# Kernel optimization log

Measured on AMD Instinct MI355X. Metric: run time of the kernel, lower is better.

Reference implementation:

```python
import jax, jax.numpy as jnp
import numpy as np

B, N, DIN, D, L, H = 8, 1024, 768, 384, 6, 12
HD = D // H
STD = 0.02
EPS = 1e-5


def setup_inputs() -> dict:
    key = jax.random.key(0)
    ks = jax.random.split(key, 24)
    inp = {}
    inp["x"] = jax.random.normal(ks[0], (B, N, DIN), jnp.float32)
    inp["height_ids"] = jax.random.randint(ks[1], (B, N), 0, 48)
    inp["width_ids"] = jax.random.randint(ks[2], (B, N), 0, 48)
    inp["target_mask"] = jax.random.randint(ks[3], (B, N), 0, 2).astype(bool)
    inp["sequence_ids"] = jnp.sort(jax.random.randint(ks[4], (B, N), 0, 8), axis=-1)
    inp["sequence_mask"] = (jax.random.randint(ks[5], (B, N), 0, 10) > 8)
    inp["r"] = 0
    # parameters (weights stored [in, out]; y = x @ W + b)
    inp["embed_w"] = jax.random.normal(ks[6], (DIN, D), jnp.float32) * STD
    inp["embed_b"] = jnp.zeros((D,), jnp.float32)
    inp["h_embed"] = jax.random.normal(ks[7], (48, D), jnp.float32) * STD
    inp["w_embed"] = jax.random.normal(ks[8], (48, D), jnp.float32) * STD
    inp["mask_token"] = jax.random.normal(ks[9], (D,), jnp.float32) * STD
    rescale = (1.0 / jnp.sqrt(2.0 * (jnp.arange(L) + 1.0))).astype(jnp.float32)
    inp["norm1_w"] = jnp.ones((L, D), jnp.float32)
    inp["norm1_b"] = jnp.zeros((L, D), jnp.float32)
    inp["ls1"] = 1e-5 * jnp.ones((L, D), jnp.float32)
    inp["qkv_w"] = jax.random.normal(ks[10], (L, D, 3 * D), jnp.float32) * STD
    inp["qkv_b"] = jnp.zeros((L, 3 * D), jnp.float32)
    inp["proj_w"] = jax.random.normal(ks[11], (L, D, D), jnp.float32) * STD * rescale[:, None, None]
    inp["proj_b"] = jnp.zeros((L, D), jnp.float32)
    inp["norm2_w"] = jnp.ones((L, D), jnp.float32)
    inp["norm2_b"] = jnp.zeros((L, D), jnp.float32)
    inp["fc1_w"] = jax.random.normal(ks[12], (L, D, 4 * D), jnp.float32) * STD
    inp["fc1_b"] = jnp.zeros((L, 4 * D), jnp.float32)
    inp["fc2_w"] = jax.random.normal(ks[13], (L, 4 * D, D), jnp.float32) * STD * rescale[:, None, None]
    inp["fc2_b"] = jnp.zeros((L, D), jnp.float32)
    inp["ls2"] = 1e-5 * jnp.ones((L, D), jnp.float32)
    inp["pnorm_w"] = jnp.ones((D,), jnp.float32)
    inp["pnorm_b"] = jnp.zeros((D,), jnp.float32)
    inp["pproj_w"] = jax.random.normal(ks[14], (D, DIN), jnp.float32) * STD
    inp["pproj_b"] = jnp.zeros((DIN,), jnp.float32)
    return inp


def _layernorm(x, w, b):
    mu = jnp.mean(x, axis=-1, keepdims=True)
    var = jnp.mean(jnp.square(x - mu), axis=-1, keepdims=True)
    return (x - mu) * jax.lax.rsqrt(var + EPS) * w + b


def _attention(x, attn_mask, qkv_w, qkv_b, proj_w, proj_b):
    # x: [B,N,D]; attn_mask: [B,1,N,N] True where attention is disallowed
    qkv = (x @ qkv_w + qkv_b).reshape(B, N, 3, H, HD).transpose(2, 0, 3, 1, 4)
    q, k, v = qkv[0], qkv[1], qkv[2]  # [B,H,N,HD]
    attn = jnp.einsum("bhnd,bhmd->bhnm", q, k) * (HD ** -0.5)
    neg_inf = jnp.finfo(attn.dtype).min
    attn = jnp.where(attn_mask, neg_inf, attn)
    attn = jax.nn.softmax(attn, axis=-1)
    out = jnp.einsum("bhnm,bhmd->bhnd", attn, v).transpose(0, 2, 1, 3).reshape(B, N, D)
    return out @ proj_w + proj_b


def reference(x, height_ids, width_ids, target_mask, sequence_ids, sequence_mask, r,
              embed_w, embed_b, h_embed, w_embed, mask_token,
              norm1_w, norm1_b, ls1, qkv_w, qkv_b, proj_w, proj_b,
              norm2_w, norm2_b, fc1_w, fc1_b, fc2_w, fc2_b, ls2,
              pnorm_w, pnorm_b, pproj_w, pproj_b):
    h = x @ embed_w + embed_b
    tm = target_mask[..., None]
    h = jnp.where(tm, mask_token, h)
    h = h + h_embed[height_ids] + w_embed[width_ids]
    # packed-sequence block-diagonal mask; True = NOT allowed
    mask = sequence_ids[:, :, None] != sequence_ids[:, None, :]
    mask = mask | sequence_mask[:, :, None] | sequence_mask[:, None, :]
    mask = mask[:, None]  # broadcast over heads: [B,1,N,N]
    for i in range(L):  # r == 0 path: plain blocks, tome is None
        h = h + ls1[i] * _attention(_layernorm(h, norm1_w[i], norm1_b[i]), mask,
                                    qkv_w[i], qkv_b[i], proj_w[i], proj_b[i])
        z = _layernorm(h, norm2_w[i], norm2_b[i])
        z = jax.nn.gelu(z @ fc1_w[i] + fc1_b[i], approximate=False) @ fc2_w[i] + fc2_b[i]
        h = h + ls2[i] * z
    h = _layernorm(h, pnorm_w, pnorm_b)
    return h @ pproj_w + pproj_b
```

## Files before the change

kernel.cpp:

```cpp
#include <hip/hip_runtime.h>
#include <math.h>

#define BB   8
#define NN   1024
#define DIN  768
#define DD   384
#define LL   6
#define HH   12
#define HDD  32
#define MM   (BB*NN)
#define EPSF 1e-5f

typedef __attribute__((ext_vector_type(8))) short short8;
typedef __attribute__((ext_vector_type(4))) float f32x4;

__device__ __forceinline__ unsigned short f2b(float f) {
    unsigned int u = __builtin_bit_cast(unsigned int, f);
    u = (u + 0x7fffu + ((u >> 16) & 1u)) >> 16;
    return (unsigned short)u;
}
__device__ __forceinline__ float b2f(unsigned short h) {
    return __builtin_bit_cast(float, ((unsigned int)h) << 16);
}

__global__ __launch_bounds__(1024) void cvt_mask_k(const void* __restrict__ src,
                                                   int n, int* __restrict__ dst)
{
    __shared__ int flag;
    if (threadIdx.x == 0) flag = 0;
    __syncthreads();
    const int* si = (const int*)src;
    int nq = n >> 2;
    int any = 0;
    for (int i = threadIdx.x; i < nq; i += blockDim.x) any |= si[i] & ~1;
    if (any) atomicOr(&flag, 1);
    __syncthreads();
    if (flag) {
        const unsigned char* sb = (const unsigned char*)src;
        for (int i = threadIdx.x; i < n; i += blockDim.x) dst[i] = sb[i];
    } else {
        for (int i = threadIdx.x; i < n; i += blockDim.x) dst[i] = si[i];
    }
}

__global__ __launch_bounds__(256) void split_k(const float* __restrict__ X,
                                               unsigned short* __restrict__ Xh,
                                               unsigned short* __restrict__ Xl,
                                               int n4)
{
    int i = blockIdx.x * 256 + threadIdx.x;
    int stride = gridDim.x * 256;
    for (; i < n4; i += stride) {
        float4 v = ((const float4*)X)[i];
        ushort4 h4, l4;
        #pragma unroll
        for (int e = 0; e < 4; ++e) {
            float f = ((const float*)&v)[e];
            unsigned short hi = f2b(f);
            ((unsigned short*)&h4)[e] = hi;
            ((unsigned short*)&l4)[e] = f2b(f - b2f(hi));
        }
        ((ushort4*)Xh)[i] = h4;
        ((ushort4*)Xl)[i] = l4;
    }
}

__global__ __launch_bounds__(64) void kminmax_k(const int* __restrict__ sids,
                                                const int* __restrict__ smask,
                                                int2* __restrict__ kmm)
{
    int e = blockIdx.x;
    int b = e >> 4, kt = e & 15;
    int lane = threadIdx.x;
    int kk = b * NN + kt * 64 + lane;
    int s = sids[kk];
    int msk = smask[kk];
    int mn = msk ? 0x7fffffff : s;
    int mx = msk ? (int)0x80000000 : s;
    #pragma unroll
    for (int off = 32; off; off >>= 1) {
        mn = min(mn, __shfl_xor(mn, off));
        mx = max(mx, __shfl_xor(mx, off));
    }
    if (lane == 0) kmm[e] = make_int2(mn, mx);
}

__global__ __launch_bounds__(256) void vmean_k(const unsigned short* __restrict__ qkv,
                                               unsigned short* __restrict__ vmean)
{
    __shared__ float part[8][32];
    int bh = blockIdx.x;
    int b = bh / HH, h = bh % HH;
    int d = threadIdx.x & 31, grp = threadIdx.x >> 5;
    const unsigned short* vp = qkv + (size_t)(b * NN + grp * 128) * (3 * DD)
                                   + 2 * DD + h * HDD + d;
    float s = 0.f;
    for (int n = 0; n < 128; ++n)
        s += b2f(vp[(size_t)n * 3 * DD]);
    part[grp][d] = s;
    __syncthreads();
    if (grp == 0) {
        float t = 0.f;
        #pragma unroll
        for (int g2 = 0; g2 < 8; ++g2) t += part[g2][d];
        vmean[bh * HDD + d] = f2b(t * (1.0f / NN));
    }
}

__global__ __launch_bounds__(256) void tcast_k(const float* __restrict__ W,
                                               unsigned short* __restrict__ Wt,
                                               int K, int N)
{
    __shared__ float tile[32][33];
    const size_t lstr = (size_t)K * N;
    const float* Wl = W + blockIdx.z * lstr;
    unsigned short* Wtl = Wt + blockIdx.z * lstr;
    int k0 = blockIdx.x * 32, n0 = blockIdx.y * 32;
    int tx = threadIdx.x & 31, ty = threadIdx.x >> 5;
    #pragma unroll
    for (int r = 0; r < 32; r += 8)
        tile[ty + r][tx] = Wl[(size_t)(k0 + ty + r) * N + n0 + tx];
    __syncthreads();
    #pragma unroll
    for (int r = 0; r < 32; r += 8)
        Wtl[(size_t)(n0 + ty + r) * K + k0 + tx] = f2b(tile[tx][ty + r]);
}

__global__ __launch_bounds__(256) void tcast2_k(const float* __restrict__ W,
                                                unsigned short* __restrict__ WTh,
                                                unsigned short* __restrict__ WTl,
                                                int K, int N)
{
    __shared__ float tile[32][33];
    int k0 = blockIdx.x * 32, n0 = blockIdx.y * 32;
    int tx = threadIdx.x & 31, ty = threadIdx.x >> 5;
    #pragma unroll
    for (int r = 0; r < 32; r += 8)
        tile[ty + r][tx] = W[(size_t)(k0 + ty + r) * N + n0 + tx];
    __syncthreads();
    #pragma unroll
    for (int r = 0; r < 32; r += 8) {
        float v = tile[tx][ty + r];
        unsigned short hi = f2b(v);
        unsigned short lo = f2b(v - b2f(hi));
        size_t idx = (size_t)(n0 + ty + r) * K + k0 + tx;
        WTh[idx] = hi;
        WTl[idx] = lo;
    }
}

template <int EPI>
__global__ __launch_bounds__(256) void sgemm_k(
    const unsigned short* __restrict__ Agh, const unsigned short* __restrict__ Agl,
    const unsigned short* __restrict__ WTh, const unsigned short* __restrict__ WTl,
    const float* __restrict__ bias, float* __restrict__ out,
    int K, int NO,
    const int* __restrict__ tmask, const int* __restrict__ hids,
    const int* __restrict__ wids, const float* __restrict__ mtok,
    const float* __restrict__ hemb, const float* __restrict__ wemb)
{
    __shared__ unsigned short Ah[128][40];
    __shared__ unsigned short Al[128][40];
    __shared__ unsigned short Bh[64][40];
    __shared__ unsigned short Bl[64][40];

    const int tid  = threadIdx.x;
    const int lane = tid & 63;
    const int wave = tid >> 6;
    const int wr = wave >> 1, wc = wave & 1;
    const int rowBase = blockIdx.x * 128;
    const int colBase = blockIdx.y * 64;
    const int rr = lane & 15;
    const int kr = (lane >> 4) * 8;

    f32x4 acc[4][2] = {};

    for (int k0 = 0; k0 < K; k0 += 32) {
        #pragma unroll
        for (int i = 0; i < 2; ++i) {
            int s   = tid + i * 256;
            int row = s >> 2;
            int seg = (s & 3) * 8;
            size_t gi = (size_t)(rowBase + row) * K + k0 + seg;
            *(short8*)&Ah[row][seg] = *(const short8*)&Agh[gi];
            *(short8*)&Al[row][seg] = *(const short8*)&Agl[gi];
        }
        {
            int row = tid >> 2;
            int seg = (tid & 3) * 8;
            size_t gi = (size_t)(colBase + row) * K + k0 + seg;
            *(short8*)&Bh[row][seg] = *(const short8*)&WTh[gi];
            *(short8*)&Bl[row][seg] = *(const short8*)&WTl[gi];
        }
        __syncthreads();

        short8 ah[4], al[4], bh2[2], bl2[2];
        #pragma unroll
        for (int i = 0; i < 4; ++i) {
            ah[i] = *(const short8*)&Ah[wr * 64 + i * 16 + rr][kr];
            al[i] = *(const short8*)&Al[wr * 64 + i * 16 + rr][kr];
        }
        #pragma unroll
        for (int j = 0; j < 2; ++j) {
            bh2[j] = *(const short8*)&Bh[wc * 32 + j * 16 + rr][kr];
            bl2[j] = *(const short8*)&Bl[wc * 32 + j * 16 + rr][kr];
        }
        #pragma unroll
        for (int i = 0; i < 4; ++i)
            #pragma unroll
            for (int j = 0; j < 2; ++j) {
                acc[i][j] = __builtin_amdgcn_mfma_f32_16x16x32_bf16(
                    al[i], bh2[j], acc[i][j], 0, 0, 0);
                acc[i][j] = __builtin_amdgcn_mfma_f32_16x16x32_bf16(
                    ah[i], bl2[j], acc[i][j], 0, 0, 0);
                acc[i][j] = __builtin_amdgcn_mfma_f32_16x16x32_bf16(
                    ah[i], bh2[j], acc[i][j], 0, 0, 0);
            }
        __syncthreads();
    }

    const int colq = colBase + wc * 32 + rr;
    const int rq0  = rowBase + wr * 64 + (lane >> 4) * 4;
    #pragma unroll
    for (int j = 0; j < 2; ++j) {
        const int col = colq + j * 16;
        const float bi = bias[col];
        #pragma unroll
        for (int i = 0; i < 4; ++i) {
            #pragma unroll
            for (int r = 0; r < 4; ++r) {
                const int row = rq0 + i * 16 + r;
                float v = acc[i][j][r] + bi;
                if constexpr (EPI == 1) {
                    float xv = tmask[row] ? mtok[col] : v;
                    out[(size_t)row * NO + col] = xv
                        + hemb[(size_t)hids[row] * DD + col]
                        + wemb[(size_t)wids[row] * DD + col];
                } else {
                    out[(size_t)row * NO + col] = v;
                }
            }
        }
    }
}

template <int EPI>
__global__ __launch_bounds__(256) void bgemm_k(
    const unsigned short* __restrict__ A, const unsigned short* __restrict__ Wt,
    const float* __restrict__ bias, void* __restrict__ out,
    int K, int NO, const float* __restrict__ ls)
{
    __shared__ unsigned short As[128][40];
    __shared__ unsigned short Bs[128][40];

    const int tid  = threadIdx.x;
    const int lane = tid & 63;
    const int wave = tid >> 6;
    const int wr = wave >> 1, wc = wave & 1;
    const int rowBase = blockIdx.x * 128;
    const int colBase = blockIdx.y * 128;
    const int rr = lane & 15;
    const int kr = (lane >> 4) * 8;

    f32x4 acc[4][4] = {};

    for (int k0 = 0; k0 < K; k0 += 32) {
        #pragma unroll
        for (int i = 0; i < 2; ++i) {
            int s   = tid + i * 256;
            int row = s >> 2;
            int seg = (s & 3) * 8;
            *(short8*)&As[row][seg] =
                *(const short8*)&A[(size_t)(rowBase + row) * K + k0 + seg];
            *(short8*)&Bs[row][seg] =
                *(const short8*)&Wt[(size_t)(colBase + row) * K + k0 + seg];
        }
        __syncthreads();

        short8 af[4], bfr[4];
        #pragma unroll
        for (int i = 0; i < 4; ++i)
            af[i] = *(const short8*)&As[wr * 64 + i * 16 + rr][kr];
        #pragma unroll
        for (int j = 0; j < 4; ++j)
            bfr[j] = *(const short8*)&Bs[wc * 64 + j * 16 + rr][kr];
        #pragma unroll
        for (int i = 0; i < 4; ++i)
            #pragma unroll
            for (int j = 0; j < 4; ++j)
                acc[i][j] = __builtin_amdgcn_mfma_f32_16x16x32_bf16(
                    af[i], bfr[j], acc[i][j], 0, 0, 0);
        __syncthreads();
    }

    const int colq = colBase + wc * 64 + rr;
    const int rq0  = rowBase + wr * 64 + (lane >> 4) * 4;
    #pragma unroll
    for (int j = 0; j < 4; ++j) {
        const int col = colq + j * 16;
        const float bi = bias[col];
        #pragma unroll
        for (int i = 0; i < 4; ++i) {
            #pragma unroll
            for (int r = 0; r < 4; ++r) {
                const int row = rq0 + i * 16 + r;
                float v = acc[i][j][r] + bi;
                if constexpr (EPI == 0) {
                    ((unsigned short*)out)[(size_t)row * NO + col] = f2b(v);
                } else {
                    float g = 0.5f * v * (1.0f + erff(v * 0.70710678118654752f));
                    ((unsigned short*)out)[(size_t)row * NO + col] = f2b(g);
                }
            }
        }
    }
}

__global__ __launch_bounds__(256) void bgemm64_k(
    const unsigned short* __restrict__ A, const unsigned short* __restrict__ Wt,
    const float* __restrict__ bias, float* __restrict__ h,
    int K, int NO, const float* __restrict__ ls)
{
    __shared__ unsigned short As[64][40];
    __shared__ unsigned short Bs[64][40];

    const int tid  = threadIdx.x;
    const int lane = tid & 63;
    const int wave = tid >> 6;
    const int wr = wave >> 1, wc = wave & 1;
    const int rowBase = blockIdx.x * 64;
    const int colBase = blockIdx.y * 64;
    const int rr = lane & 15;
    const int kr = (lane >> 4) * 8;

    f32x4 acc[2][2] = {};

    for (int k0 = 0; k0 < K; k0 += 32) {
        {
            int row = tid >> 2;
            int seg = (tid & 3) * 8;
            *(short8*)&As[row][seg] =
                *(const short8*)&A[(size_t)(rowBase + row) * K + k0 + seg];
            *(short8*)&Bs[row][seg] =
                *(const short8*)&Wt[(size_t)(colBase + row) * K + k0 + seg];
        }
        __syncthreads();

        short8 af[2], bfr[2];
        #pragma unroll
        for (int i = 0; i < 2; ++i)
            af[i] = *(const short8*)&As[wr * 32 + i * 16 + rr][kr];
        #pragma unroll
        for (int j = 0; j < 2; ++j)
            bfr[j] = *(const short8*)&Bs[wc * 32 + j * 16 + rr][kr];
        #pragma unroll
        for (int i = 0; i < 2; ++i)
            #pragma unroll
            for (int j = 0; j < 2; ++j)
                acc[i][j] = __builtin_amdgcn_mfma_f32_16x16x32_bf16(
                    af[i], bfr[j], acc[i][j], 0, 0, 0);
        __syncthreads();
    }

    const int colq = colBase + wc * 32 + rr;
    const int rq0  = rowBase + wr * 32 + (lane >> 4) * 4;
    #pragma unroll
    for (int j = 0; j < 2; ++j) {
        const int col = colq + j * 16;
        const float bi = bias[col];
        const float lsv = ls[col];
        #pragma unroll
        for (int i = 0; i < 2; ++i) {
            #pragma unroll
            for (int r = 0; r < 4; ++r) {
                const int row = rq0 + i * 16 + r;
                float* hp = &h[(size_t)row * NO + col];
                *hp += lsv * (acc[i][j][r] + bi);
            }
        }
    }
}

template <int OUT>
__global__ __launch_bounds__(256) void ln_k(
    const float* __restrict__ X, const float* __restrict__ w,
    const float* __restrict__ b, void* __restrict__ Y, void* __restrict__ Yl)
{
    int row  = blockIdx.x * 4 + (threadIdx.x >> 6);
    int lane = threadIdx.x & 63;
    const float* xr = X + (size_t)row * DD;

    float2 x2[3];
    #pragma unroll
    for (int j = 0; j < 3; ++j)
        x2[j] = *(const float2*)&xr[2 * (lane + 64 * j)];

    float s = 0.f;
    #pragma unroll
    for (int j = 0; j < 3; ++j) s += x2[j].x + x2[j].y;
    #pragma unroll
    for (int off = 32; off > 0; off >>= 1) s += __shfl_xor(s, off);
    float mu = s * (1.0f / 384.0f);

    float v = 0.f;
    #pragma unroll
    for (int j = 0; j < 3; ++j) {
        float d0 = x2[j].x - mu, d1 = x2[j].y - mu;
        v += d0 * d0 + d1 * d1;
    }
    #pragma unroll
    for (int off = 32; off > 0; off >>= 1) v += __shfl_xor(v, off);
    float rstd = rsqrtf(v * (1.0f / 384.0f) + EPSF);

    #pragma unroll
    for (int j = 0; j < 3; ++j) {
        int c = 2 * (lane + 64 * j);
        float2 w2 = *(const float2*)&w[c];
        float2 b2 = *(const float2*)&b[c];
        float y0 = (x2[j].x - mu) * rstd * w2.x + b2.x;
        float y1 = (x2[j].y - mu) * rstd * w2.y + b2.y;
        unsigned short h0 = f2b(y0), h1 = f2b(y1);
        *(ushort2*)&((unsigned short*)Y)[(size_t)row * DD + c] = make_ushort2(h0, h1);
        if constexpr (OUT == 2) {
            unsigned short l0 = f2b(y0 - b2f(h0)), l1 = f2b(y1 - b2f(h1));
            *(ushort2*)&((unsigned short*)Yl)[(size_t)row * DD + c] = make_ushort2(l0, l1);
        }
    }
}

__global__ __launch_bounds__(256) void attn_mfma_k(
    const unsigned short* __restrict__ qkv, const int* __restrict__ sids,
    const int* __restrict__ smask, const int2* __restrict__ kmm,
    const unsigned short* __restrict__ vmean, unsigned short* __restrict__ out)
{
    __shared__ unsigned short Vt[32][72];
    __shared__ int ck[64];
    __shared__ unsigned short P[4][16][64];
    __shared__ int qmn[4], qmx[4];

    const int tid  = threadIdx.x;
    const int lane = tid & 63;
    const int wave = tid >> 6;
    const int g = lane >> 4;
    const int c = lane & 15;

    const int bh = blockIdx.x >> 4;
    const int qt = blockIdx.x & 15;
    const int b = bh / HH, h = bh % HH;
    const int q0w = qt * 64 + wave * 16;
    const size_t qrow = 3 * DD;

    const short8 qf = *(const short8*)&qkv[(size_t)(b * NN + q0w + c) * qrow + h * HDD + g * 8];

    int cq[4];
    #pragma unroll
    for (int r = 0; r < 4; ++r) {
        int qq = b * NN + q0w + 4 * g + r;
        cq[r] = smask[qq] ? -2 : sids[qq];
    }

    {
        int lmin = 0x7fffffff, lmax = (int)0x80000000;
        #pragma unroll
        for (int r = 0; r < 4; ++r) {
            if (cq[r] != -2) { lmin = min(lmin, cq[r]); lmax = max(lmax, cq[r]); }
        }
        #pragma unroll
        for (int off = 32; off; off >>= 1) {
            lmin = min(lmin, __shfl_xor(lmin, off));
            lmax = max(lmax, __shfl_xor(lmax, off));
        }
        if (lane == 0) { qmn[wave] = lmin; qmx[wave] = lmax; }
    }
    __syncthreads();
    int qminb = min(min(qmn[0], qmn[1]), min(qmn[2], qmn[3]));
    int qmaxb = max(max(qmx[0], qmx[1]), max(qmx[2], qmx[3]));

    float m[4] = {-INFINITY, -INFINITY, -INFINITY, -INFINITY};
    float l[4] = {};
    f32x4 o[2] = {};
    const f32x4 zero = {};
    const float scale = 0.17677669529663687f;
    const float FMIN = -3.402823466e38f;

    for (int kt = 0; kt < NN / 64; ++kt) {
        const int2 kr2 = kmm[(b << 4) + kt];
        if (kr2.x > qmaxb || kr2.y < qminb) continue;

        const int kb = kt * 64;
        {
            int key = tid & 63;
            int d8  = (tid >> 6) * 8;
            short8 v = *(const short8*)&qkv[(size_t)(b * NN + kb + key) * qrow + 2 * DD + h * HDD + d8];
            #pragma unroll
            for (int e = 0; e < 8; ++e)
                Vt[d8 + e][key] = (unsigned short)v[e];
            if (tid < 64) {
                int kk = b * NN + kb + tid;
                ck[tid] = smask[kk] ? -1 : sids[kk];
            }
        }
        __syncthreads();

        f32x4 s4[4];
        #pragma unroll
        for (int j = 0; j < 4; ++j) {
            short8 kf = *(const short8*)&qkv[(size_t)(b * NN + kb + 16 * j + c) * qrow + DD + h * HDD + g * 8];
            s4[j] = __builtin_amdgcn_mfma_f32_16x16x32_bf16(qf, kf, zero, 0, 0, 0);
        }

        float pm[4] = {FMIN, FMIN, FMIN, FMIN};
        #pragma unroll
        for (int j = 0; j < 4; ++j) {
            const int ckj = ck[16 * j + c];
            #pragma unroll
            for (int r = 0; r < 4; ++r) {
                float sv = (cq[r] != ckj) ? FMIN : s4[j][r] * scale;
                s4[j][r] = sv;
                pm[r] = fmaxf(pm[r], sv);
            }
        }
        #pragma unroll
        for (int off = 1; off < 16; off <<= 1)
            #pragma unroll
            for (int r = 0; r < 4; ++r)
                pm[r] = fmaxf(pm[r], __shfl_xor(pm[r], off));

        float fac[4], psum[4];
        #pragma unroll
        for (int r = 0; r < 4; ++r) {
            float mn = fmaxf(m[r], pm[r]);
            fac[r] = __expf(m[r] - mn);
            m[r] = mn;
            psum[r] = 0.f;
        }
        #pragma unroll
        for (int j = 0; j < 4; ++j) {
            #pragma unroll
            for (int r = 0; r < 4; ++r) {
                float p = __expf(s4[j][r] - m[r]);
                psum[r] += p;
                int row  = 4 * g + r;
                int colb = (2 * (16 * j + c)) ^ ((row & 7) << 4);
                *(unsigned short*)((char*)&P[wave][row][0] + colb) = f2b(p);
            }
        }
        #pragma unroll
        for (int off = 1; off < 16; off <<= 1)
            #pragma unroll
            for (int r = 0; r < 4; ++r)
                psum[r] += __shfl_xor(psum[r], off);
        #pragma unroll
        for (int r = 0; r < 4; ++r) l[r] = l[r] * fac[r] + psum[r];

        #pragma unroll
        for (int dc = 0; dc < 2; ++dc)
            #pragma unroll
            for (int r = 0; r < 4; ++r)
                o[dc][r] *= fac[r];

        #pragma unroll
        for (int kc = 0; kc < 2; ++kc) {
            int colb = (2 * (kc * 32 + g * 8)) ^ ((c & 7) << 4);
            short8 pf = *(const short8*)((char*)&P[wave][c][0] + colb);
            #pragma unroll
            for (int dc = 0; dc < 2; ++dc) {
                short8 vf = *(const short8*)&Vt[dc * 16 + c][kc * 32 + g * 8];
                o[dc] = __builtin_amdgcn_mfma_f32_16x16x32_bf16(pf, vf, o[dc], 0, 0, 0);
            }
        }
        __syncthreads();
    }

    #pragma unroll
    for (int r = 0; r < 4; ++r) {
        unsigned short* op = &out[(size_t)(b * NN + q0w + 4 * g + r) * DD + h * HDD];
        if (cq[r] == -2) {
            #pragma unroll
            for (int dc = 0; dc < 2; ++dc)
                op[dc * 16 + c] = vmean[bh * HDD + dc * 16 + c];
        } else {
            const float inv = 1.0f / l[r];
            #pragma unroll
            for (int dc = 0; dc < 2; ++dc)
                op[dc * 16 + c] = f2b(o[dc][r] * inv);
        }
    }
}

extern "C" void kernel_launch(void* const* d_in, const int* in_sizes, int n_in,
                              void* d_out, int out_size, void* d_ws, size_t ws_size,
                              hipStream_t stream)
{
    const float* x        = (const float*)d_in[0];
    const int*   hids     = (const int*)d_in[1];
    const int*   wids     = (const int*)d_in[2];
    const void*  tmask_rw = d_in[3];
    const int*   sids     = (const int*)d_in[4];
    const void*  smask_rw = d_in[5];
    const float* embed_w  = (const float*)d_in[7];
    const float* embed_b  = (const float*)d_in[8];
    const float* h_embed  = (const float*)d_in[9];
    const float* w_embed  = (const float*)d_in[10];
    const float* mtok     = (const float*)d_in[11];
    const float* norm1_w  = (const float*)d_in[12];
    const float* norm1_b  = (const float*)d_in[13];
    const float* ls1      = (const float*)d_in[14];
    const float* qkv_w    = (const float*)d_in[15];
    const float* qkv_b    = (const float*)d_in[16];
    const float* proj_w   = (const float*)d_in[17];
    const float* proj_b   = (const float*)d_in[18];
    const float* norm2_w  = (const float*)d_in[19];
    const float* norm2_b  = (const float*)d_in[20];
    const float* fc1_w    = (const float*)d_in[21];
    const float* fc1_b    = (const float*)d_in[22];
    const float* fc2_w    = (const float*)d_in[23];
    const float* fc2_b    = (const float*)d_in[24];
    const float* ls2      = (const float*)d_in[25];
    const float* pnorm_w  = (const float*)d_in[26];
    const float* pnorm_b  = (const float*)d_in[27];
    const float* pproj_w  = (const float*)d_in[28];
    const float* pproj_b  = (const float*)d_in[29];

    const size_t MD = (size_t)MM * DD;
    float*          h    = (float*)d_ws;
    unsigned short* zb   = (unsigned short*)(h + MD);
    unsigned short* hid  = zb + MD;
    unsigned short* qkvb = hid;
    unsigned short* zfh  = hid;
    unsigned short* zfl  = hid + MD;
    const size_t xsz = (size_t)MM * DIN;
    unsigned short* xh = hid;
    unsigned short* xl = hid + xsz;
    unsigned short* wT   = hid + 4 * MD;
    const size_t qkvTsz  = (size_t)LL * 3 * DD * DD;
    const size_t projTsz = (size_t)LL * DD * DD;
    const size_t fc1Tsz  = (size_t)LL * DD * 4 * DD;
    unsigned short* qkvT = wT;
    unsigned short* projT = qkvT + qkvTsz;
    unsigned short* fc1T  = projT + projTsz;
    unsigned short* fc2T  = fc1T + fc1Tsz;
    int* tm32 = (int*)(fc2T + fc1Tsz);
    int* sm32 = tm32 + MM;
    unsigned short* vmean = (unsigned short*)(sm32 + MM);
    int2* kmm = (int2*)(vmean + BB * HH * HDD);
    const size_t ewsz = (size_t)DIN * DD;
    unsigned short* ewT_hi = (unsigned short*)(kmm + BB * 16);
    unsigned short* ewT_lo = ewT_hi + ewsz;
    unsigned short* pwT_hi = ewT_lo + ewsz;
    unsigned short* pwT_lo = pwT_hi + ewsz;

    cvt_mask_k<<<1, 1024, 0, stream>>>(tmask_rw, MM, tm32);
    cvt_mask_k<<<1, 1024, 0, stream>>>(smask_rw, MM, sm32);
    kminmax_k<<<BB * 16, 64, 0, stream>>>(sids, sm32, kmm);

    dim3 t256(256);
    tcast_k<<<dim3(DD/32, 3*DD/32, LL), t256, 0, stream>>>(qkv_w, qkvT, DD, 3*DD);
    tcast_k<<<dim3(DD/32, DD/32,   LL), t256, 0, stream>>>(proj_w, projT, DD, DD);
    tcast_k<<<dim3(DD/32, 4*DD/32, LL), t256, 0, stream>>>(fc1_w, fc1T, DD, 4*DD);
    tcast_k<<<dim3(4*DD/32, DD/32, LL), t256, 0, stream>>>(fc2_w, fc2T, 4*DD, DD);
    tcast2_k<<<dim3(DIN/32, DD/32), t256, 0, stream>>>(embed_w, ewT_hi, ewT_lo, DIN, DD);
    tcast2_k<<<dim3(DD/32, DIN/32), t256, 0, stream>>>(pproj_w, pwT_hi, pwT_lo, DD, DIN);
    split_k<<<2048, t256, 0, stream>>>(x, xh, xl, (int)(xsz / 4));

    sgemm_k<1><<<dim3(MM/128, DD/64), t256, 0, stream>>>(
        xh, xl, ewT_hi, ewT_lo, embed_b, h, DIN, DD, tm32, hids, wids, mtok, h_embed, w_embed);

    for (int i = 0; i < LL; ++i) {
        ln_k<1><<<MM/4, t256, 0, stream>>>(h, norm1_w + i*DD, norm1_b + i*DD, zb, nullptr);
        bgemm_k<0><<<dim3(MM/128, 3*DD/128), t256, 0, stream>>>(
            zb, qkvT + (size_t)i*3*DD*DD, qkv_b + i*3*DD, qkvb, DD, 3*DD, nullptr);
        vmean_k<<<BB * HH, t256, 0, stream>>>(qkvb, vmean);
        attn_mfma_k<<<dim3(BB*HH*(NN/64)), t256, 0, stream>>>(
            qkvb, sids, sm32, kmm, vmean, zb);
        bgemm64_k<<<dim3(MM/64, DD/64), t256, 0, stream>>>(
            zb, projT + (size_t)i*DD*DD, proj_b + i*DD, h, DD, DD, ls1 + i*DD);
        ln_k<1><<<MM/4, t256, 0, stream>>>(h, norm2_w + i*DD, norm2_b + i*DD, zb, nullptr);
        bgemm_k<3><<<dim3(MM/128, 4*DD/128), t256, 0, stream>>>(
            zb, fc1T + (size_t)i*DD*4*DD, fc1_b + i*4*DD, hid, DD, 4*DD, nullptr);
        bgemm64_k<<<dim3(MM/64, DD/64), t256, 0, stream>>>(
            hid, fc2T + (size_t)i*4*DD*DD, fc2_b + i*DD, h, 4*DD, DD, ls2 + i*DD);
    }

    ln_k<2><<<MM/4, t256, 0, stream>>>(h, pnorm_w, pnorm_b, zfh, zfl);
    sgemm_k<0><<<dim3(MM/128, DIN/64), t256, 0, stream>>>(
        zfh, zfl, pwT_hi, pwT_lo, pproj_b, (float*)d_out, DD, DIN,
        nullptr, nullptr, nullptr, nullptr, nullptr, nullptr);
}
```

Measured before the change: 1.115 ms.

## Write QKV in head-major layout from GEMM epilogue for contiguous attention loads

The QKV GEMM epilogue now scatters its output into three separate [B,H,N,32] planes (Q, K, V) instead of a row-major [M,3D] buffer. The attention and V-mean kernels then read each head's K/V rows contiguously (64-byte rows) rather than striding by 3*D elements. This is meant to improve coalescing and cache-line use in the attention inner loop. The cost is that the GEMM epilogue's scattered per-element stores are less regular.

New measurement: 1.124 ms. Within noise of the previous version (+0.8%).

```diff
diff --git a/kernel.cpp b/kernel.cpp
--- a/kernel.cpp
+++ b/kernel.cpp
@@ -10,6 +10,7 @@
 #define HDD  32
 #define MM   (BB*NN)
 #define EPSF 1e-5f
+#define PS   ((size_t)BB*HH*NN*HDD)
 
 typedef __attribute__((ext_vector_type(8))) short short8;
 typedef __attribute__((ext_vector_type(4))) float f32x4;
@@ -85,18 +86,16 @@
     if (lane == 0) kmm[e] = make_int2(mn, mx);
 }
 
-__global__ __launch_bounds__(256) void vmean_k(const unsigned short* __restrict__ qkv,
+__global__ __launch_bounds__(256) void vmean_k(const unsigned short* __restrict__ Vh,
                                                unsigned short* __restrict__ vmean)
 {
     __shared__ float part[8][32];
     int bh = blockIdx.x;
-    int b = bh / HH, h = bh % HH;
     int d = threadIdx.x & 31, grp = threadIdx.x >> 5;
-    const unsigned short* vp = qkv + (size_t)(b * NN + grp * 128) * (3 * DD)
-                                   + 2 * DD + h * HDD + d;
+    const unsigned short* vp = Vh + ((size_t)bh * NN + grp * 128) * HDD + d;
     float s = 0.f;
     for (int n = 0; n < 128; ++n)
-        s += b2f(vp[(size_t)n * 3 * DD]);
+        s += b2f(vp[n * HDD]);
     part[grp][d] = s;
     __syncthreads();
     if (grp == 0) {
@@ -307,6 +306,13 @@
                 float v = acc[i][j][r] + bi;
                 if constexpr (EPI == 0) {
                     ((unsigned short*)out)[(size_t)row * NO + col] = f2b(v);
+                } else if constexpr (EPI == 4) {
+                    int part = col / DD;
+                    int rem  = col - part * DD;
+                    int hh   = rem >> 5, hd = rem & 31;
+                    int b    = row >> 10, n = row & (NN - 1);
+                    ((unsigned short*)out)[part * PS +
+                        (((size_t)(b * HH + hh) * NN + n) << 5) + hd] = f2b(v);
                 } else {
                     float g = 0.5f * v * (1.0f + erff(v * 0.70710678118654752f));
                     ((unsigned short*)out)[(size_t)row * NO + col] = f2b(g);
@@ -429,7 +435,7 @@
 }
 
 __global__ __launch_bounds__(256) void attn_mfma_k(
-    const unsigned short* __restrict__ qkv, const int* __restrict__ sids,
+    const unsigned short* __restrict__ qs, const int* __restrict__ sids,
     const int* __restrict__ smask, const int2* __restrict__ kmm,
     const unsigned short* __restrict__ vmean, unsigned short* __restrict__ out)
 {
@@ -448,9 +454,13 @@
     const int qt = blockIdx.x & 15;
     const int b = bh / HH, h = bh % HH;
     const int q0w = qt * 64 + wave * 16;
-    const size_t qrow = 3 * DD;
-
-    const short8 qf = *(const short8*)&qkv[(size_t)(b * NN + q0w + c) * qrow + h * HDD + g * 8];
+
+    const unsigned short* Qh = qs;
+    const unsigned short* Kh = qs + PS;
+    const unsigned short* Vh = qs + 2 * PS;
+    const size_t hb = (size_t)bh * NN * HDD;
+
+    const short8 qf = *(const short8*)&Qh[hb + (size_t)(q0w + c) * HDD + g * 8];
 
     int cq[4];
     #pragma unroll
@@ -491,7 +501,7 @@
         {
             int key = tid & 63;
             int d8  = (tid >> 6) * 8;
-            short8 v = *(const short8*)&qkv[(size_t)(b * NN + kb + key) * qrow + 2 * DD + h * HDD + d8];
+            short8 v = *(const short8*)&Vh[hb + (size_t)(kb + key) * HDD + d8];
             #pragma unroll
             for (int e = 0; e < 8; ++e)
                 Vt[d8 + e][key] = (unsigned short)v[e];
@@ -505,7 +515,7 @@
         f32x4 s4[4];
         #pragma unroll
         for (int j = 0; j < 4; ++j) {
-            short8 kf = *(const short8*)&qkv[(size_t)(b * NN + kb + 16 * j + c) * qrow + DD + h * HDD + g * 8];
+            short8 kf = *(const short8*)&Kh[hb + (size_t)(kb + 16 * j + c) * HDD + g * 8];
             s4[j] = __builtin_amdgcn_mfma_f32_16x16x32_bf16(qf, kf, zero, 0, 0, 0);
         }
 
@@ -626,7 +636,7 @@
     float*          h    = (float*)d_ws;
     unsigned short* zb   = (unsigned short*)(h + MD);
     unsigned short* hid  = zb + MD;
-    unsigned short* qkvb = hid;
+    unsigned short* qkvs = hid;
     unsigned short* zfh  = hid;
     unsigned short* zfl  = hid + MD;
     const size_t xsz = (size_t)MM * DIN;
@@ -668,11 +678,11 @@
 
     for (int i = 0; i < LL; ++i) {
         ln_k<1><<<MM/4, t256, 0, stream>>>(h, norm1_w + i*DD, norm1_b + i*DD, zb, nullptr);
-        bgemm_k<0><<<dim3(MM/128, 3*DD/128), t256, 0, stream>>>(
-            zb, qkvT + (size_t)i*3*DD*DD, qkv_b + i*3*DD, qkvb, DD, 3*DD, nullptr);
-        vmean_k<<<BB * HH, t256, 0, stream>>>(qkvb, vmean);
+        bgemm_k<4><<<dim3(MM/128, 3*DD/128), t256, 0, stream>>>(
+            zb, qkvT + (size_t)i*3*DD*DD, qkv_b + i*3*DD, qkvs, DD, 3*DD, nullptr);
+        vmean_k<<<BB * HH, t256, 0, stream>>>(qkvs + 2 * MD, vmean);
         attn_mfma_k<<<dim3(BB*HH*(NN/64)), t256, 0, stream>>>(
-            qkvb, sids, sm32, kmm, vmean, zb);
+            qkvs, sids, sm32, kmm, vmean, zb);
         bgemm64_k<<<dim3(MM/64, DD/64), t256, 0, stream>>>(
             zb, projT + (size_t)i*DD*DD, proj_b + i*DD, h, DD, DD, ls1 + i*DD);
         ln_k<1><<<MM/4, t256, 0, stream>>>(h, norm2_w + i*DD, norm2_b + i*DD, zb, nullptr);
```
